# Kernel tuning notes

Measured on AMD Instinct MI355X. Metric: run time of the kernel, lower is better.

The kernel has to match this reference:

```python
import jax, jax.numpy as jnp
import numpy as np

B, S, H = 4, 256, 768
NUM_BASIC = 4
NUM_REL = 32            # labels 1..31 are real edges, 0 = no edge
NUM_ALL = 2 * NUM_REL   # bidir: forward slots 0..31, reverse slots 33..63


def setup_inputs() -> dict:
    key = jax.random.key(0)
    k1, k2, k3, k4, k5 = jax.random.split(key, 5)
    hidden_states = jax.random.normal(k1, (B, S, H), dtype=jnp.float32)
    rels = jax.random.randint(k2, (B, S, S), 0, NUM_REL, dtype=jnp.int32)
    # xavier-ish init scale for params
    basic_matrix = jax.random.normal(k3, (NUM_BASIC, H, H), dtype=jnp.float32) * 0.02
    rel_weight = jax.random.normal(k4, (NUM_ALL, NUM_BASIC), dtype=jnp.float32) * 0.1
    self_weight = jax.random.normal(k5, (H, H), dtype=jnp.float32) * 0.02  # Linear weight (out,in)
    return {"hidden_states": hidden_states, "rels": rels,
            "basic_matrix": basic_matrix, "rel_weight": rel_weight,
            "self_weight": self_weight}


def reference(hidden_states, rels, basic_matrix, rel_weight, self_weight):
    dt = hidden_states.dtype
    # forward-direction one-hot relation tensor [B, NUM_ALL, S, S], masked where rels == 0
    fwd_mask = (rels > 0).astype(dt)                                   # [B,S,S]
    fwd_oh = jax.nn.one_hot(rels, NUM_ALL, axis=1, dtype=dt) * fwd_mask[:, None]
    # reverse direction (bidir): labels shifted by NUM_REL, zeroed where no edge
    rev_rels_raw = jnp.transpose(rels, (0, 2, 1))
    rev_rels = jnp.where(rev_rels_raw > 0, rev_rels_raw + NUM_REL, 0)  # {0} U {33..63}
    rev_mask = (rev_rels > 0).astype(dt)
    rev_oh = jax.nn.one_hot(rev_rels, NUM_ALL, axis=1, dtype=dt) * rev_mask[:, None]
    rel_tensor = fwd_oh + rev_oh                                       # [B,R,S,S]

    # basis decomposition: per-relation transform [R, H, H]
    rel_matrix = jnp.einsum('rb,bio->rio', rel_weight, basic_matrix)
    # per-relation transformed hidden states [B,R,S,H]
    r_hidden = jnp.einsum('bsi,rio->brso', hidden_states, rel_matrix)
    # adjacency aggregation [B,R,S,H]
    r_ctx = jnp.einsum('brij,brjo->brio', rel_tensor, r_hidden)
    # mean over neighbors (clamp count at 1)
    num_neighbors = jnp.maximum(rel_tensor.sum(-1), 1.0)               # [B,R,S]
    r_ctx = r_ctx / num_neighbors[..., None]
    context = r_ctx.sum(axis=1)                                        # [B,S,H]
    self_layer = hidden_states @ self_weight.T
    return self_layer + context
```

## Files before the change

kernel.cpp:

```cpp
#include <hip/hip_runtime.h>
#include <stdint.h>

typedef unsigned short u16;
typedef unsigned int u32;
typedef __attribute__((ext_vector_type(8))) short short8;
typedef __attribute__((ext_vector_type(4))) float float4v;

#define Bb 4
#define Ss 256
#define Hh 768
#define NALL 64


__device__ __forceinline__ float b2f(u16 h) {
    u32 u = ((u32)h) << 16;
    float f;
    __builtin_memcpy(&f, &u, 4);
    return f;
}
__device__ __forceinline__ u16 f2b(float f) {
    u32 u;
    __builtin_memcpy(&u, &f, 4);
    u = (u + 0x7fffu + ((u >> 16) & 1u)) >> 16;
    return (u16)u;
}

__global__ __launch_bounds__(256) void k_prep(const float* __restrict__ h,
                                              const int* __restrict__ rels,
                                              const float* __restrict__ basic,
                                              const float* __restrict__ relw,
                                              const float* __restrict__ selfw,
                                              u16* __restrict__ basicT,
                                              u16* __restrict__ coefC,
                                              u16* __restrict__ hbf,
                                              u16* __restrict__ swbf) {
    __shared__ u16 tile[32][34];
    __shared__ float srelw[256];
    __shared__ u32 hist[NALL];
    const int z = blockIdx.x;
    const int t = threadIdx.x;

    if (z < 2304) {
        const int q = z / 576, rem = z % 576;
        const int i0 = (rem % 24) * 32, o0 = (rem / 24) * 32;
        const int tx = t & 31, ty = t >> 5;
        const size_t base = (size_t)q * Hh * Hh;
#pragma unroll
        for (int r = 0; r < 4; ++r)
            tile[ty + 8 * r][tx] = f2b(basic[base + (size_t)(i0 + ty + 8 * r) * Hh + o0 + tx]);
        __syncthreads();
#pragma unroll
        for (int r = 0; r < 4; ++r)
            basicT[base + (size_t)(o0 + ty + 8 * r) * Hh + i0 + tx] = tile[tx][ty + 8 * r];
    } else if (z < 3328) {
        const int r = z - 2304;
        const int i = r & 255, b = r >> 8;
        srelw[t] = relw[t];
        if (t < NALL) hist[t] = 0u;
        __syncthreads();
        const int rfw = rels[(b * Ss + i) * Ss + t];
        const int rcl = rels[(b * Ss + t) * Ss + i];
        if (rfw > 0) atomicAdd(&hist[rfw], 1u);
        if (rcl > 0) atomicAdd(&hist[rcl + 32], 1u);
        __syncthreads();
        float c0 = 0.f, c1 = 0.f, c2 = 0.f, c3 = 0.f;
        if (rfw > 0) {
            const float inv = 1.0f / (float)hist[rfw];
            c0 += srelw[rfw * 4 + 0] * inv; c1 += srelw[rfw * 4 + 1] * inv;
            c2 += srelw[rfw * 4 + 2] * inv; c3 += srelw[rfw * 4 + 3] * inv;
        }
        if (rcl > 0) {
            const int rr = rcl + 32;
            const float inv = 1.0f / (float)hist[rr];
            c0 += srelw[rr * 4 + 0] * inv; c1 += srelw[rr * 4 + 1] * inv;
            c2 += srelw[rr * 4 + 2] * inv; c3 += srelw[rr * 4 + 3] * inv;
        }
        const size_t base = ((size_t)(b * 4) * Ss + i) * Ss + t;
        coefC[base] = f2b(c0);
        coefC[base + (size_t)Ss * Ss] = f2b(c1);
        coefC[base + (size_t)2 * Ss * Ss] = f2b(c2);
        coefC[base + (size_t)3 * Ss * Ss] = f2b(c3);
    } else if (z < 4096) {
        const size_t i = ((size_t)(z - 3328) * 256 + t) * 4;
        const float4 v = *(const float4*)(h + i);
        u32 lo = (u32)f2b(v.x) | ((u32)f2b(v.y) << 16);
        u32 hi = (u32)f2b(v.z) | ((u32)f2b(v.w) << 16);
        *(uint2*)(hbf + i) = make_uint2(lo, hi);
    } else {
        const size_t i = ((size_t)(z - 4096) * 256 + t) * 4;
        const float4 v = *(const float4*)(selfw + i);
        u32 lo = (u32)f2b(v.x) | ((u32)f2b(v.y) << 16);
        u32 hi = (u32)f2b(v.z) | ((u32)f2b(v.w) << 16);
        *(uint2*)(swbf + i) = make_uint2(lo, hi);
    }
}

__global__ __launch_bounds__(256, 4) void k_mid(const u16* __restrict__ basicT,
                                                const u16* __restrict__ hbf,
                                                u16* __restrict__ Gt) {
    __shared__ __align__(16) u16 As[64 * 72];
    __shared__ __align__(16) u16 Bs[64 * 72];
    const int z = blockIdx.x;
    const int o0 = (z % 12) * 64, j0 = ((z / 12) % 4) * 64, bk = z / 48;
    const int b = bk >> 2, q = bk & 3;
    const int t = threadIdx.x;
    const int row = t >> 2, kk = (t & 3) * 16;
    const int w = t >> 6, l = t & 63, quad = l >> 4, l16 = l & 15;

    const u16* aB = basicT + ((size_t)q * Hh + o0 + row) * Hh + kk;
    const u16* bB = hbf + ((size_t)b * Ss + j0 + row) * Hh + kk;

    float4v acc[4];
#pragma unroll
    for (int c = 0; c < 4; ++c) acc[c] = (float4v){0.f, 0.f, 0.f, 0.f};
    uint4 a0 = *(const uint4*)aB, a1 = *(const uint4*)(aB + 8);
    uint4 b0 = *(const uint4*)bB, b1 = *(const uint4*)(bB + 8);

    for (int s = 0; s < 12; ++s) {
        __syncthreads();
        *(uint4*)(&As[row * 72 + kk]) = a0;
        *(uint4*)(&As[row * 72 + kk + 8]) = a1;
        *(uint4*)(&Bs[row * 72 + kk]) = b0;
        *(uint4*)(&Bs[row * 72 + kk + 8]) = b1;
        __syncthreads();
        if (s + 1 < 12) {
            a0 = *(const uint4*)(aB + (s + 1) * 64);
            a1 = *(const uint4*)(aB + (s + 1) * 64 + 8);
            b0 = *(const uint4*)(bB + (s + 1) * 64);
            b1 = *(const uint4*)(bB + (s + 1) * 64 + 8);
        }
#pragma unroll
        for (int k2 = 0; k2 < 64; k2 += 32) {
            const short8 af = *(const short8*)(&As[(16 * w + l16) * 72 + k2 + quad * 8]);
#pragma unroll
            for (int c = 0; c < 4; ++c) {
                const short8 bfr = *(const short8*)(&Bs[(16 * c + l16) * 72 + k2 + quad * 8]);
                acc[c] = __builtin_amdgcn_mfma_f32_16x16x32_bf16(af, bfr, acc[c], 0, 0, 0);
            }
        }
    }

#pragma unroll
    for (int c = 0; c < 4; ++c)
#pragma unroll
        for (int r = 0; r < 4; ++r) {
            const int ol = 16 * w + quad * 4 + r;
            const int jl = 16 * c + l16;
            Gt[((size_t)bk * Hh + o0 + ol) * Ss + j0 + jl] = f2b(acc[c][r]);
        }
}

__global__ __launch_bounds__(256, 4) void k_phase2(const u16* __restrict__ coefC,
                                                   const u16* __restrict__ Gt,
                                                   const u16* __restrict__ hbf,
                                                   const u16* __restrict__ swbf,
                                                   float* __restrict__ out) {
    __shared__ __align__(16) u16 As[64 * 72];
    __shared__ __align__(16) u16 Bs[64 * 72];
    const int z = blockIdx.x;
    const int ot = z % 12, it = (z / 12) % 4, b = z / 48;
    const int t = threadIdx.x;
    const int row = t >> 2, kk = (t & 3) * 16;
    const int w = t >> 6, l = t & 63, quad = l >> 4, l16 = l & 15;

    auto aa = [&](int s) -> const u16* {
        if (s < 16)
            return coefC + ((size_t)(b * 4 + (s >> 2)) * Ss + it * 64 + row) * Ss + (s & 3) * 64 + kk;
        return hbf + ((size_t)b * Ss + it * 64 + row) * Hh + (s - 16) * 64 + kk;
    };
    auto bb = [&](int s) -> const u16* {
        if (s < 16)
            return Gt + ((size_t)(b * 4 + (s >> 2)) * Hh + ot * 64 + row) * Ss + (s & 3) * 64 + kk;
        return swbf + (size_t)(ot * 64 + row) * Hh + (s - 16) * 64 + kk;
    };

    float4v acc[4];
#pragma unroll
    for (int c = 0; c < 4; ++c) acc[c] = (float4v){0.f, 0.f, 0.f, 0.f};
    uint4 a0 = *(const uint4*)aa(0);
    uint4 a1 = *(const uint4*)(aa(0) + 8);
    uint4 b0 = *(const uint4*)bb(0);
    uint4 b1 = *(const uint4*)(bb(0) + 8);

    for (int s = 0; s < 28; ++s) {
        __syncthreads();
        *(uint4*)(&As[row * 72 + kk]) = a0;
        *(uint4*)(&As[row * 72 + kk + 8]) = a1;
        *(uint4*)(&Bs[row * 72 + kk]) = b0;
        *(uint4*)(&Bs[row * 72 + kk + 8]) = b1;
        __syncthreads();
        if (s + 1 < 28) {
            const u16* ap = aa(s + 1);
            const u16* bp = bb(s + 1);
            a0 = *(const uint4*)ap;
            a1 = *(const uint4*)(ap + 8);
            b0 = *(const uint4*)bp;
            b1 = *(const uint4*)(bp + 8);
        }
#pragma unroll
        for (int k2 = 0; k2 < 64; k2 += 32) {
            const short8 af = *(const short8*)(&As[(16 * w + l16) * 72 + k2 + quad * 8]);
#pragma unroll
            for (int c = 0; c < 4; ++c) {
                const short8 bfr = *(const short8*)(&Bs[(16 * c + l16) * 72 + k2 + quad * 8]);
                acc[c] = __builtin_amdgcn_mfma_f32_16x16x32_bf16(af, bfr, acc[c], 0, 0, 0);
            }
        }
    }

#pragma unroll
    for (int c = 0; c < 4; ++c)
#pragma unroll
        for (int r = 0; r < 4; ++r) {
            const int il = 16 * w + quad * 4 + r;
            const int ol = 16 * c + l16;
            out[((size_t)b * Ss + it * 64 + il) * Hh + ot * 64 + ol] = acc[c][r];
        }
}

extern "C" void kernel_launch(void* const* d_in, const int* in_sizes, int n_in,
                              void* d_out, int out_size, void* d_ws, size_t ws_size,
                              hipStream_t stream) {
    const float* h = (const float*)d_in[0];
    const int* rels = (const int*)d_in[1];
    const float* basic = (const float*)d_in[2];
    const float* relw = (const float*)d_in[3];
    const float* selfw = (const float*)d_in[4];
    float* out = (float*)d_out;

    u16* basicT = (u16*)d_ws;
    u16* coefC = basicT + (size_t)4 * Hh * Hh;
    u16* Gt = coefC + (size_t)Bb * 4 * Ss * Ss;
    u16* hbf = Gt + (size_t)Bb * 4 * Hh * Ss;
    u16* swbf = hbf + (size_t)Bb * Ss * Hh;

    k_prep<<<4672, 256, 0, stream>>>(h, rels, basic, relw, selfw, basicT, coefC, hbf, swbf);
    k_mid<<<768, 256, 0, stream>>>(basicT, hbf, Gt);
    k_phase2<<<192, 256, 0, stream>>>(coefC, Gt, hbf, swbf, out);
}
```

Measured before the change: 102.8 us.

## Move self-linear GEMM into mid kernel and use 2x2 warp tiling

```diff
diff --git a/kernel.cpp b/kernel.cpp
--- a/kernel.cpp
+++ b/kernel.cpp
@@ -97,63 +97,87 @@
 
 __global__ __launch_bounds__(256, 4) void k_mid(const u16* __restrict__ basicT,
                                                 const u16* __restrict__ hbf,
-                                                u16* __restrict__ Gt) {
+                                                const u16* __restrict__ swbf,
+                                                u16* __restrict__ Gt,
+                                                float* __restrict__ out) {
     __shared__ __align__(16) u16 As[64 * 72];
     __shared__ __align__(16) u16 Bs[64 * 72];
     const int z = blockIdx.x;
-    const int o0 = (z % 12) * 64, j0 = ((z / 12) % 4) * 64, bk = z / 48;
-    const int b = bk >> 2, q = bk & 3;
     const int t = threadIdx.x;
     const int row = t >> 2, kk = (t & 3) * 16;
     const int w = t >> 6, l = t & 63, quad = l >> 4, l16 = l & 15;
-
-    const u16* aB = basicT + ((size_t)q * Hh + o0 + row) * Hh + kk;
-    const u16* bB = hbf + ((size_t)b * Ss + j0 + row) * Hh + kk;
-
-    float4v acc[4];
-#pragma unroll
-    for (int c = 0; c < 4; ++c) acc[c] = (float4v){0.f, 0.f, 0.f, 0.f};
-    uint4 a0 = *(const uint4*)aB, a1 = *(const uint4*)(aB + 8);
-    uint4 b0 = *(const uint4*)bB, b1 = *(const uint4*)(bB + 8);
+    const int wr = (w >> 1) * 32, wc = (w & 1) * 32;
+
+    const bool selfF = (z >= 768);
+    const u16* aB;
+    const u16* bB;
+    size_t stBase;
+    if (!selfF) {
+        const int o0 = (z % 12) * 64, j0 = ((z / 12) % 4) * 64, bk = z / 48;
+        const int b = bk >> 2, q = bk & 3;
+        aB = basicT + ((size_t)q * Hh + o0 + row) * Hh + kk;
+        bB = hbf + ((size_t)b * Ss + j0 + row) * Hh + kk;
+        stBase = ((size_t)bk * Hh + o0) * Ss + j0;
+    } else {
+        const int zz = z - 768;
+        const int ot = zz % 12, it = (zz / 12) % 4, b = zz / 48;
+        aB = hbf + ((size_t)b * Ss + it * 64 + row) * Hh + kk;
+        bB = swbf + (size_t)(ot * 64 + row) * Hh + kk;
+        stBase = ((size_t)b * Ss + it * 64) * Hh + ot * 64;
+    }
+
+    float4v acc[2][2];
+#pragma unroll
+    for (int m = 0; m < 2; ++m)
+#pragma unroll
+        for (int n = 0; n < 2; ++n) acc[m][n] = (float4v){0.f, 0.f, 0.f, 0.f};
+    uint4 sa0 = *(const uint4*)aB, sa1 = *(const uint4*)(aB + 8);
+    uint4 sb0 = *(const uint4*)bB, sb1 = *(const uint4*)(bB + 8);
 
     for (int s = 0; s < 12; ++s) {
         __syncthreads();
-        *(uint4*)(&As[row * 72 + kk]) = a0;
-        *(uint4*)(&As[row * 72 + kk + 8]) = a1;
-        *(uint4*)(&Bs[row * 72 + kk]) = b0;
-        *(uint4*)(&Bs[row * 72 + kk + 8]) = b1;
+        *(uint4*)(&As[row * 72 + kk]) = sa0;
+        *(uint4*)(&As[row * 72 + kk + 8]) = sa1;
+        *(uint4*)(&Bs[row * 72 + kk]) = sb0;
+        *(uint4*)(&Bs[row * 72 + kk + 8]) = sb1;
         __syncthreads();
         if (s + 1 < 12) {
-            a0 = *(const uint4*)(aB + (s + 1) * 64);
-            a1 = *(const uint4*)(aB + (s + 1) * 64 + 8);
-            b0 = *(const uint4*)(bB + (s + 1) * 64);
-            b1 = *(const uint4*)(bB + (s + 1) * 64 + 8);
+            sa0 = *(const uint4*)(aB + (s + 1) * 64);
+            sa1 = *(const uint4*)(aB + (s + 1) * 64 + 8);
+            sb0 = *(const uint4*)(bB + (s + 1) * 64);
+            sb1 = *(const uint4*)(bB + (s + 1) * 64 + 8);
         }
 #pragma unroll
         for (int k2 = 0; k2 < 64; k2 += 32) {
-            const short8 af = *(const short8*)(&As[(16 * w + l16) * 72 + k2 + quad * 8]);
-#pragma unroll
-            for (int c = 0; c < 4; ++c) {
-                const short8 bfr = *(const short8*)(&Bs[(16 * c + l16) * 72 + k2 + quad * 8]);
-                acc[c] = __builtin_amdgcn_mfma_f32_16x16x32_bf16(af, bfr, acc[c], 0, 0, 0);
+            const int ko = k2 + quad * 8;
+            const short8 fa0 = *(const short8*)(&As[(wr + l16) * 72 + ko]);
+            const short8 fa1 = *(const short8*)(&As[(wr + 16 + l16) * 72 + ko]);
+            const short8 fb0 = *(const short8*)(&Bs[(wc + l16) * 72 + ko]);
+            const short8 fb1 = *(const short8*)(&Bs[(wc + 16 + l16) * 72 + ko]);
+            acc[0][0] = __builtin_amdgcn_mfma_f32_16x16x32_bf16(fa0, fb0, acc[0][0], 0, 0, 0);
+            acc[0][1] = __builtin_amdgcn_mfma_f32_16x16x32_bf16(fa0, fb1, acc[0][1], 0, 0, 0);
+            acc[1][0] = __builtin_amdgcn_mfma_f32_16x16x32_bf16(fa1, fb0, acc[1][0], 0, 0, 0);
+            acc[1][1] = __builtin_amdgcn_mfma_f32_16x16x32_bf16(fa1, fb1, acc[1][1], 0, 0, 0);
+        }
+    }
+
+#pragma unroll
+    for (int m = 0; m < 2; ++m)
+#pragma unroll
+        for (int n = 0; n < 2; ++n)
+#pragma unroll
+            for (int r = 0; r < 4; ++r) {
+                const int rowl = wr + 16 * m + quad * 4 + r;
+                const int coll = wc + 16 * n + l16;
+                if (!selfF)
+                    Gt[stBase + (size_t)rowl * Ss + coll] = f2b(acc[m][n][r]);
+                else
+                    out[stBase + (size_t)rowl * Hh + coll] = acc[m][n][r];
             }
-        }
-    }
-
-#pragma unroll
-    for (int c = 0; c < 4; ++c)
-#pragma unroll
-        for (int r = 0; r < 4; ++r) {
-            const int ol = 16 * w + quad * 4 + r;
-            const int jl = 16 * c + l16;
-            Gt[((size_t)bk * Hh + o0 + ol) * Ss + j0 + jl] = f2b(acc[c][r]);
-        }
 }
 
 __global__ __launch_bounds__(256, 4) void k_phase2(const u16* __restrict__ coefC,
                                                    const u16* __restrict__ Gt,
-                                                   const u16* __restrict__ hbf,
-                                                   const u16* __restrict__ swbf,
                                                    float* __restrict__ out) {
     __shared__ __align__(16) u16 As[64 * 72];
     __shared__ __align__(16) u16 Bs[64 * 72];
@@ -162,60 +186,67 @@
     const int t = threadIdx.x;
     const int row = t >> 2, kk = (t & 3) * 16;
     const int w = t >> 6, l = t & 63, quad = l >> 4, l16 = l & 15;
+    const int wr = (w >> 1) * 32, wc = (w & 1) * 32;
+    const int b4 = b * 4, i0 = it * 64, o0 = ot * 64;
 
     auto aa = [&](int s) -> const u16* {
-        if (s < 16)
-            return coefC + ((size_t)(b * 4 + (s >> 2)) * Ss + it * 64 + row) * Ss + (s & 3) * 64 + kk;
-        return hbf + ((size_t)b * Ss + it * 64 + row) * Hh + (s - 16) * 64 + kk;
+        return coefC + ((size_t)(b4 + (s >> 2)) * Ss + i0 + row) * Ss + (s & 3) * 64 + kk;
     };
     auto bb = [&](int s) -> const u16* {
-        if (s < 16)
-            return Gt + ((size_t)(b * 4 + (s >> 2)) * Hh + ot * 64 + row) * Ss + (s & 3) * 64 + kk;
-        return swbf + (size_t)(ot * 64 + row) * Hh + (s - 16) * 64 + kk;
+        return Gt + ((size_t)(b4 + (s >> 2)) * Hh + o0 + row) * Ss + (s & 3) * 64 + kk;
     };
-
-    float4v acc[4];
-#pragma unroll
-    for (int c = 0; c < 4; ++c) acc[c] = (float4v){0.f, 0.f, 0.f, 0.f};
-    uint4 a0 = *(const uint4*)aa(0);
-    uint4 a1 = *(const uint4*)(aa(0) + 8);
-    uint4 b0 = *(const uint4*)bb(0);
-    uint4 b1 = *(const uint4*)(bb(0) + 8);
-
-    for (int s = 0; s < 28; ++s) {
-        __syncthreads();
-        *(uint4*)(&As[row * 72 + kk]) = a0;
-        *(uint4*)(&As[row * 72 + kk + 8]) = a1;
-        *(uint4*)(&Bs[row * 72 + kk]) = b0;
-        *(uint4*)(&Bs[row * 72 + kk + 8]) = b1;
-        __syncthreads();
-        if (s + 1 < 28) {
+    const size_t stBase = ((size_t)b * Ss + i0) * Hh + o0;
+
+    float4v acc[2][2];
+#pragma unroll
+    for (int m = 0; m < 2; ++m)
+#pragma unroll
+        for (int n = 0; n < 2; ++n) acc[m][n] = (float4v){0.f, 0.f, 0.f, 0.f};
+    uint4 sa0 = *(const uint4*)aa(0);
+    uint4 sa1 = *(const uint4*)(aa(0) + 8);
+    uint4 sb0 = *(const uint4*)bb(0);
+    uint4 sb1 = *(const uint4*)(bb(0) + 8);
+
+    for (int s = 0; s < 16; ++s) {
+        __syncthreads();
+        *(uint4*)(&As[row * 72 + kk]) = sa0;
+        *(uint4*)(&As[row * 72 + kk + 8]) = sa1;
+        *(uint4*)(&Bs[row * 72 + kk]) = sb0;
+        *(uint4*)(&Bs[row * 72 + kk + 8]) = sb1;
+        __syncthreads();
+        if (s + 1 < 16) {
             const u16* ap = aa(s + 1);
             const u16* bp = bb(s + 1);
-            a0 = *(const uint4*)ap;
-            a1 = *(const uint4*)(ap + 8);
-            b0 = *(const uint4*)bp;
-            b1 = *(const uint4*)(bp + 8);
+            sa0 = *(const uint4*)ap;
+            sa1 = *(const uint4*)(ap + 8);
+            sb0 = *(const uint4*)bp;
+            sb1 = *(const uint4*)(bp + 8);
         }
 #pragma unroll
         for (int k2 = 0; k2 < 64; k2 += 32) {
-            const short8 af = *(const short8*)(&As[(16 * w + l16) * 72 + k2 + quad * 8]);
-#pragma unroll
-            for (int c = 0; c < 4; ++c) {
-                const short8 bfr = *(const short8*)(&Bs[(16 * c + l16) * 72 + k2 + quad * 8]);
-                acc[c] = __builtin_amdgcn_mfma_f32_16x16x32_bf16(af, bfr, acc[c], 0, 0, 0);
+            const int ko = k2 + quad * 8;
+            const short8 fa0 = *(const short8*)(&As[(wr + l16) * 72 + ko]);
+            const short8 fa1 = *(const short8*)(&As[(wr + 16 + l16) * 72 + ko]);
+            const short8 fb0 = *(const short8*)(&Bs[(wc + l16) * 72 + ko]);
+            const short8 fb1 = *(const short8*)(&Bs[(wc + 16 + l16) * 72 + ko]);
+            acc[0][0] = __builtin_amdgcn_mfma_f32_16x16x32_bf16(fa0, fb0, acc[0][0], 0, 0, 0);
+            acc[0][1] = __builtin_amdgcn_mfma_f32_16x16x32_bf16(fa0, fb1, acc[0][1], 0, 0, 0);
+            acc[1][0] = __builtin_amdgcn_mfma_f32_16x16x32_bf16(fa1, fb0, acc[1][0], 0, 0, 0);
+            acc[1][1] = __builtin_amdgcn_mfma_f32_16x16x32_bf16(fa1, fb1, acc[1][1], 0, 0, 0);
+        }
+    }
+
+#pragma unroll
+    for (int m = 0; m < 2; ++m)
+#pragma unroll
+        for (int n = 0; n < 2; ++n)
+#pragma unroll
+            for (int r = 0; r < 4; ++r) {
+                const int rowl = wr + 16 * m + quad * 4 + r;
+                const int coll = wc + 16 * n + l16;
+                const size_t idx = stBase + (size_t)rowl * Hh + coll;
+                out[idx] += acc[m][n][r];
             }
-        }
-    }
-
-#pragma unroll
-    for (int c = 0; c < 4; ++c)
-#pragma unroll
-        for (int r = 0; r < 4; ++r) {
-            const int il = 16 * w + quad * 4 + r;
-            const int ol = 16 * c + l16;
-            out[((size_t)b * Ss + it * 64 + il) * Hh + ot * 64 + ol] = acc[c][r];
-        }
 }
 
 extern "C" void kernel_launch(void* const* d_in, const int* in_sizes, int n_in,
@@ -235,6 +266,6 @@
     u16* swbf = hbf + (size_t)Bb * Ss * Hh;
 
     k_prep<<<4672, 256, 0, stream>>>(h, rels, basic, relw, selfw, basicT, coefC, hbf, swbf);
-    k_mid<<<768, 256, 0, stream>>>(basicT, hbf, Gt);
-    k_phase2<<<192, 256, 0, stream>>>(coefC, Gt, hbf, swbf, out);
-}
+    k_mid<<<960, 256, 0, stream>>>(basicT, hbf, swbf, Gt, out);
+    k_phase2<<<192, 256, 0, stream>>>(coefC, Gt, out);
+}
```

After: 103.2 us. Within noise of the previous version (+0.4%).
